# Performance work log

Hardware: AMD Instinct MI355X
Metric: run time of the kernel (lower is better)

Reference implementation:

```python
import jax, jax.numpy as jnp
import numpy as np

N = 50000   # nodes
E = 600000  # edges
D = 128     # in_feats
H = 128     # n_hidden
C = 47      # n_classes


def setup_inputs() -> dict:
    key = jax.random.key(0)
    ks = jax.random.split(key, 12)
    x = jax.random.normal(ks[0], (N, D), dtype=jnp.float32)
    src = jax.random.randint(ks[1], (E,), 0, N, dtype=jnp.int32)
    dst = jax.random.randint(ks[2], (E,), 0, N, dtype=jnp.int32)
    def lin(k, fi, fo):
        s = 1.0 / np.sqrt(fi)
        return jax.random.uniform(k, (fi, fo), jnp.float32, -s, s)
    return {
        "x": x, "src": src, "dst": dst,
        "W_self0": lin(ks[3], D, H), "W_neigh0": lin(ks[4], D, H), "b0": jnp.zeros((H,), jnp.float32),
        "W_self1": lin(ks[5], H, H), "W_neigh1": lin(ks[6], H, H), "b1": jnp.zeros((H,), jnp.float32),
        "W_self2": lin(ks[7], H, C), "W_neigh2": lin(ks[8], H, C), "b2": jnp.zeros((C,), jnp.float32),
    }


def _sage_layer(h, src, dst, W_self, W_neigh, b, act):
    # gather neighbor (src) features, mean-aggregate onto dst nodes
    msum = jax.ops.segment_sum(h[src], dst, num_segments=N)           # [N, F]
    deg = jax.ops.segment_sum(jnp.ones((src.shape[0], 1), h.dtype), dst, num_segments=N)
    h_neigh = msum / jnp.maximum(deg, 1.0)                            # zero-degree -> 0
    out = h @ W_self + h_neigh @ W_neigh + b
    return jax.nn.relu(out) if act else out


def reference(x, src, dst, W_self0, W_neigh0, b0, W_self1, W_neigh1, b1, W_self2, W_neigh2, b2):
    h = _sage_layer(x, src, dst, W_self0, W_neigh0, b0, True)
    h = _sage_layer(h, src, dst, W_self1, W_neigh1, b1, True)
    h = _sage_layer(h, src, dst, W_self2, W_neigh2, b2, False)
    return h
```

## Files before the change

### kernel.cpp

```cpp
#include <hip/hip_runtime.h>
#include <hip/hip_bf16.h>


#define THREADS 256

typedef unsigned short u16;
typedef __attribute__((ext_vector_type(8))) short bf16x8;
typedef __attribute__((ext_vector_type(4))) float f32x4;

__device__ inline u16 f2bf(float f) {
    union { float f; unsigned u; } v; v.f = f;
    unsigned r = (v.u + 0x7FFFu + ((v.u >> 16) & 1u)) >> 16;
    return (u16)r;
}
__device__ inline float bf2f(u16 b) {
    union { unsigned u; float f; } v; v.u = ((unsigned)b) << 16;
    return v.f;
}
__device__ inline unsigned pack2(float a, float b) {
    return (unsigned)f2bf(a) | ((unsigned)f2bf(b) << 16);
}

#define GLDS16(gp, lp)                                                         \
    __builtin_amdgcn_global_load_lds(                                          \
        (const __attribute__((address_space(1))) void*)(gp),                   \
        (__attribute__((address_space(3))) void*)(lp), 16, 0, 0)

__global__ void k_preamble(const float* __restrict__ x, u16* __restrict__ hi,
                           u16* __restrict__ lo, int n32,
                           const int* __restrict__ dst, int* __restrict__ deg, int E,
                           const float* __restrict__ Ws0, const float* __restrict__ Wn0,
                           const float* __restrict__ Ws1, const float* __restrict__ Wn1,
                           const float* __restrict__ Ws2, const float* __restrict__ Wn2,
                           u16* __restrict__ Bt) {
    int idx = blockIdx.x * blockDim.x + threadIdx.x;
    if (idx < n32) {
        float4 v = ((const float4*)x)[idx];
        float h0 = bf2f(f2bf(v.x)), h1 = bf2f(f2bf(v.y)), h2 = bf2f(f2bf(v.z)), h3 = bf2f(f2bf(v.w));
        uint2 hp, lp;
        hp.x = pack2(h0, h1); hp.y = pack2(h2, h3);
        lp.x = pack2(v.x - h0, v.y - h1); lp.y = pack2(v.z - h2, v.w - h3);
        ((uint2*)hi)[idx] = hp;
        ((uint2*)lo)[idx] = lp;
    }
    if (idx < E) atomicAdd(&deg[dst[idx]], 1);
    if (idx < 3 * 128 * 256) {
        int layer = idx >> 15;
        int within = idx & 32767;
        int col = within >> 8;
        int k = within & 255;
        const float* Ws = (layer == 0) ? Ws0 : (layer == 1) ? Ws1 : Ws2;
        const float* Wn = (layer == 0) ? Wn0 : (layer == 1) ? Wn1 : Wn2;
        int fout = (layer == 2) ? 47 : 128;
        float v = 0.f;
        if (col < fout) v = (k < 128) ? Ws[k * fout + col] : Wn[(k - 128) * fout + col];
        u16 h = f2bf(v);
        Bt[layer * 65536 + within] = h;
        Bt[layer * 65536 + 32768 + within] = f2bf(v - bf2f(h));
    }
}

__global__ void k_scan_block(const int* __restrict__ deg, int* __restrict__ off,
                             int* __restrict__ bsum, int n) {
    __shared__ int s[256];
    int t = threadIdx.x;
    int base = blockIdx.x * 1024 + t * 4;
    int v[4];
#pragma unroll
    for (int i = 0; i < 4; i++) v[i] = (base + i < n) ? deg[base + i] : 0;
    int sum = v[0] + v[1] + v[2] + v[3];
    int val = sum;
    s[t] = val;
    __syncthreads();
    for (int o = 1; o < 256; o <<= 1) {
        int x = (t >= o) ? s[t - o] : 0;
        __syncthreads();
        val += x;
        s[t] = val;
        __syncthreads();
    }
    int run = val - sum;
#pragma unroll
    for (int i = 0; i < 4; i++) {
        if (base + i < n) off[base + i] = run;
        run += v[i];
    }
    if (t == 255) bsum[blockIdx.x] = val;
}

__global__ void k_scan_add(int* __restrict__ off, const int* __restrict__ bsum, int n) {
    __shared__ int sAdd;
    int t = threadIdx.x;
    if (t < 64) {
        int v = 0;
        for (int i = t; i < blockIdx.x; i += 64) v += bsum[i];
#pragma unroll
        for (int o = 32; o; o >>= 1) v += __shfl_xor(v, o, 64);
        if (t == 0) sAdd = v;
    }
    __syncthreads();
    int add = sAdd;
    int base = blockIdx.x * 1024 + t * 4;
#pragma unroll
    for (int i = 0; i < 4; i++)
        if (base + i < n) off[base + i] += add;
}

__global__ void k_fill(const int* __restrict__ src, const int* __restrict__ dst,
                       const int* __restrict__ off, int* __restrict__ cur,
                       int* __restrict__ eidx, int E) {
    int e = blockIdx.x * blockDim.x + threadIdx.x;
    if (e < E) {
        int d = dst[e];
        int p = atomicAdd(&cur[d], 1);
        eidx[off[d] + p] = src[e];
    }
}

__global__ void k_aggregate(const u16* __restrict__ hi_in, const int* __restrict__ eidx,
                            const int* __restrict__ off, const int* __restrict__ deg,
                            u16* __restrict__ mhi, u16* __restrict__ mlo, int n) {
    int wv = blockIdx.x * 4 + (threadIdx.x >> 6);
    int lane = threadIdx.x & 63;
    int quarter = lane >> 4;
    int ql = lane & 15;
    int node = wv * 4 + quarter;
    if (node >= n) return;
    int cnt = deg[node];
    int base = off[node];
    const uint4* h4 = (const uint4*)hi_in;
    float acc[8];
#pragma unroll
    for (int i = 0; i < 8; i++) acc[i] = 0.f;
    for (int j = 0; j < cnt; j += 8) {
        int s[8];
        float m[8];
#pragma unroll
        for (int u = 0; u < 8; u++) {
            int jj = j + u;
            s[u] = eidx[base + (jj < cnt ? jj : 0)];
            m[u] = (jj < cnt) ? 1.f : 0.f;
        }
        uint4 v[8];
#pragma unroll
        for (int u = 0; u < 8; u++) v[u] = h4[(size_t)s[u] * 16 + ql];
#pragma unroll
        for (int u = 0; u < 8; u++) {
            acc[0] = fmaf(m[u], bf2f((u16)(v[u].x & 0xffffu)), acc[0]);
            acc[1] = fmaf(m[u], bf2f((u16)(v[u].x >> 16)), acc[1]);
            acc[2] = fmaf(m[u], bf2f((u16)(v[u].y & 0xffffu)), acc[2]);
            acc[3] = fmaf(m[u], bf2f((u16)(v[u].y >> 16)), acc[3]);
            acc[4] = fmaf(m[u], bf2f((u16)(v[u].z & 0xffffu)), acc[4]);
            acc[5] = fmaf(m[u], bf2f((u16)(v[u].z >> 16)), acc[5]);
            acc[6] = fmaf(m[u], bf2f((u16)(v[u].w & 0xffffu)), acc[6]);
            acc[7] = fmaf(m[u], bf2f((u16)(v[u].w >> 16)), acc[7]);
        }
    }
    float iv = 1.0f / (float)(cnt > 1 ? cnt : 1);
    float a[8], r[8];
#pragma unroll
    for (int i = 0; i < 8; i++) {
        a[i] = acc[i] * iv;
        r[i] = bf2f(f2bf(a[i]));
    }
    uint4 hp, lp;
    hp.x = pack2(a[0], a[1]); hp.y = pack2(a[2], a[3]);
    hp.z = pack2(a[4], a[5]); hp.w = pack2(a[6], a[7]);
    lp.x = pack2(a[0] - r[0], a[1] - r[1]); lp.y = pack2(a[2] - r[2], a[3] - r[3]);
    lp.z = pack2(a[4] - r[4], a[5] - r[5]); lp.w = pack2(a[6] - r[6], a[7] - r[7]);
    ((uint4*)mhi)[(size_t)node * 16 + ql] = hp;
    ((uint4*)mlo)[(size_t)node * 16 + ql] = lp;
}

__global__ __launch_bounds__(256) void k_gemm_mfma(
    const u16* __restrict__ Ahi_s, const u16* __restrict__ Alo_s,
    const u16* __restrict__ Ahi_n, const u16* __restrict__ Alo_n,
    const u16* __restrict__ Bthi, const u16* __restrict__ Btlo,
    const float* __restrict__ bias, float* __restrict__ out_f32,
    u16* __restrict__ out_hi, u16* __restrict__ out_lo, int n, int fout, int relu) {
    __shared__ u16 sAhi[64 * 32];
    __shared__ u16 sAlo[64 * 32];
    __shared__ u16 sBhi[128 * 32];
    __shared__ u16 sBlo[128 * 32];

    int t = threadIdx.x;
    int w = t >> 6;
    int lane = t & 63;
    int wr = w >> 1, wc = w & 1;
    size_t row0 = (size_t)blockIdx.x * 64;

    const bool slim = (fout <= 64);
    const int rbase = slim ? (w * 16) : (wr * 32);
    const int nR = slim ? 1 : 2;
    const int cbase = slim ? 0 : (wc * 64);

    f32x4 acc[2][4];
#pragma unroll
    for (int r = 0; r < 2; r++)
#pragma unroll
        for (int c = 0; c < 4; c++) acc[r][c] = (f32x4){0.f, 0.f, 0.f, 0.f};

    for (int kk = 0; kk < 256; kk += 32) {
        const u16* Phi = (kk < 128) ? Ahi_s : Ahi_n;
        const u16* Plo = (kk < 128) ? Alo_s : Alo_n;
        int kc = kk & 127;
        __syncthreads();
        {
            int r = w * 16 + (lane >> 2);
            int cb = (lane & 3) * 8;
            GLDS16(Phi + (row0 + r) * 128 + kc + cb, &sAhi[r * 32 + cb]);
            GLDS16(Plo + (row0 + r) * 128 + kc + cb, &sAlo[r * 32 + cb]);
        }
#pragma unroll
        for (int i = 0; i < 2; i++) {
            int c = w * 32 + i * 16 + (lane >> 2);
            int cb = (lane & 3) * 8;
            GLDS16(Bthi + (size_t)c * 256 + kk + cb, &sBhi[c * 32 + cb]);
            GLDS16(Btlo + (size_t)c * 256 + kk + cb, &sBlo[c * 32 + cb]);
        }
        __syncthreads();

        bf16x8 a_hi[2], a_lo[2], b_hi[4], b_lo[4];
        int q8 = (lane >> 4) * 8;
#pragma unroll
        for (int r = 0; r < 2; r++) {
            if (r >= nR) continue;
            int ad = (rbase + r * 16 + (lane & 15)) * 32 + q8;
            a_hi[r] = *(const bf16x8*)&sAhi[ad];
            a_lo[r] = *(const bf16x8*)&sAlo[ad];
        }
#pragma unroll
        for (int c = 0; c < 4; c++) {
            int ad = (cbase + c * 16 + (lane & 15)) * 32 + q8;
            b_hi[c] = *(const bf16x8*)&sBhi[ad];
            b_lo[c] = *(const bf16x8*)&sBlo[ad];
        }
#pragma unroll
        for (int r = 0; r < 2; r++) {
            if (r >= nR) continue;
#pragma unroll
            for (int c = 0; c < 4; c++) {
                acc[r][c] = __builtin_amdgcn_mfma_f32_16x16x32_bf16(
                    a_hi[r], b_hi[c], acc[r][c], 0, 0, 0);
                acc[r][c] = __builtin_amdgcn_mfma_f32_16x16x32_bf16(
                    a_hi[r], b_lo[c], acc[r][c], 0, 0, 0);
                acc[r][c] = __builtin_amdgcn_mfma_f32_16x16x32_bf16(
                    a_lo[r], b_hi[c], acc[r][c], 0, 0, 0);
            }
        }
    }

    int quad = lane >> 4;
    int lcol = lane & 15;
#pragma unroll
    for (int r = 0; r < 2; r++) {
        if (r >= nR) continue;
#pragma unroll
        for (int c = 0; c < 4; c++) {
            int col = cbase + c * 16 + lcol;
            float bv = (col < fout) ? bias[col] : 0.f;
#pragma unroll
            for (int g = 0; g < 4; g++) {
                size_t row = row0 + rbase + r * 16 + quad * 4 + g;
                if (row >= (size_t)n || col >= fout) continue;
                float v = acc[r][c][g] + bv;
                if (relu) v = v > 0.f ? v : 0.f;
                if (out_f32) out_f32[row * fout + col] = v;
                if (out_hi) {
                    u16 h = f2bf(v);
                    out_hi[row * 128 + col] = h;
                    out_lo[row * 128 + col] = f2bf(v - bf2f(h));
                }
            }
        }
    }
}

extern "C" void kernel_launch(void* const* d_in, const int* in_sizes, int n_in,
                              void* d_out, int out_size, void* d_ws, size_t ws_size,
                              hipStream_t stream) {
    const float* x = (const float*)d_in[0];
    const int* src = (const int*)d_in[1];
    const int* dst = (const int*)d_in[2];
    const float* Ws0 = (const float*)d_in[3];
    const float* Wn0 = (const float*)d_in[4];
    const float* b0 = (const float*)d_in[5];
    const float* Ws1 = (const float*)d_in[6];
    const float* Wn1 = (const float*)d_in[7];
    const float* b1 = (const float*)d_in[8];
    const float* Ws2 = (const float*)d_in[9];
    const float* Wn2 = (const float*)d_in[10];
    const float* b2 = (const float*)d_in[11];
    float* out = (float*)d_out;

    const int N = in_sizes[0] / 128;
    const int E = in_sizes[1];
    const int Npad = ((N + 63) / 64) * 64;

    char* p = (char*)d_ws;
    u16* P0hi = (u16*)p; p += (size_t)Npad * 128 * 2;
    u16* P0lo = (u16*)p; p += (size_t)Npad * 128 * 2;
    u16* P1hi = (u16*)p; p += (size_t)Npad * 128 * 2;
    u16* P1lo = (u16*)p; p += (size_t)Npad * 128 * 2;
    u16* Mhi = (u16*)p; p += (size_t)Npad * 128 * 2;
    u16* Mlo = (u16*)p; p += (size_t)Npad * 128 * 2;
    u16* Bt = (u16*)p; p += 3 * 2 * 128 * 256 * 2;
    int* deg = (int*)p; p += (size_t)N * 4;
    int* cur = (int*)p; p += (size_t)N * 4;
    int* off = (int*)p; p += (size_t)N * 4;
    int* eidx = (int*)p; p += (size_t)E * 4;
    int* bsum = (int*)p;

    const int nPX = N * 32;
    int nPre = nPX;
    if (E > nPre) nPre = E;
    if (3 * 128 * 256 > nPre) nPre = 3 * 128 * 256;
    const int nbPre = (nPre + THREADS - 1) / THREADS;
    const int nbE = (E + THREADS - 1) / THREADS;
    const int nbScan = (N + 1023) / 1024;
    const int nbAgg = (N + 15) / 16;
    const int nbGemm = (N + 63) / 64;

    hipMemsetAsync(deg, 0, (size_t)2 * N * sizeof(int), stream);

    k_preamble<<<nbPre, THREADS, 0, stream>>>(x, P0hi, P0lo, nPX, dst, deg, E,
                                              Ws0, Wn0, Ws1, Wn1, Ws2, Wn2, Bt);
    k_scan_block<<<nbScan, 256, 0, stream>>>(deg, off, bsum, N);
    k_scan_add<<<nbScan, 256, 0, stream>>>(off, bsum, N);
    k_fill<<<nbE, THREADS, 0, stream>>>(src, dst, off, cur, eidx, E);

    k_aggregate<<<nbAgg, 256, 0, stream>>>(P0hi, eidx, off, deg, Mhi, Mlo, N);
    k_gemm_mfma<<<nbGemm, 256, 0, stream>>>(P0hi, P0lo, Mhi, Mlo,
                                            Bt + 0 * 65536, Bt + 0 * 65536 + 32768, b0,
                                            (float*)nullptr, P1hi, P1lo, N, 128, 1);
    k_aggregate<<<nbAgg, 256, 0, stream>>>(P1hi, eidx, off, deg, Mhi, Mlo, N);
    k_gemm_mfma<<<nbGemm, 256, 0, stream>>>(P1hi, P1lo, Mhi, Mlo,
                                            Bt + 1 * 65536, Bt + 1 * 65536 + 32768, b1,
                                            (float*)nullptr, P0hi, P0lo, N, 128, 1);
    k_aggregate<<<nbAgg, 256, 0, stream>>>(P0hi, eidx, off, deg, Mhi, Mlo, N);
    k_gemm_mfma<<<nbGemm, 256, 0, stream>>>(P0hi, P0lo, Mhi, Mlo,
                                            Bt + 2 * 65536, Bt + 2 * 65536 + 32768, b2,
                                            out, (u16*)nullptr, (u16*)nullptr, N, 47, 0);
}
```

Before: 299.0 us.

## Enlarge GEMM row tile to 128 and XOR-swizzle LDS layout

Doubles the rows per GEMM block from 64 to 128, so each wave computes four row fragments and each weight tile loaded into LDS is reused across twice as many rows. It also XOR-swizzles the 16-byte chunks in the shared-memory A and B tiles to reduce bank conflicts on the fragment reads. This costs more accumulator registers and more LDS per block, which may lower occupancy, and the grid has half as many blocks. Padding of the node dimension is raised to match the new tile height.

```diff
diff --git a/kernel.cpp b/kernel.cpp
--- a/kernel.cpp
+++ b/kernel.cpp
@@ -178,8 +178,8 @@
     const u16* __restrict__ Bthi, const u16* __restrict__ Btlo,
     const float* __restrict__ bias, float* __restrict__ out_f32,
     u16* __restrict__ out_hi, u16* __restrict__ out_lo, int n, int fout, int relu) {
-    __shared__ u16 sAhi[64 * 32];
-    __shared__ u16 sAlo[64 * 32];
+    __shared__ u16 sAhi[128 * 32];
+    __shared__ u16 sAlo[128 * 32];
     __shared__ u16 sBhi[128 * 32];
     __shared__ u16 sBlo[128 * 32];
 
@@ -187,56 +187,63 @@
     int w = t >> 6;
     int lane = t & 63;
     int wr = w >> 1, wc = w & 1;
-    size_t row0 = (size_t)blockIdx.x * 64;
+    size_t row0 = (size_t)blockIdx.x * 128;
 
     const bool slim = (fout <= 64);
-    const int rbase = slim ? (w * 16) : (wr * 32);
-    const int nR = slim ? 1 : 2;
+    const int rbase = slim ? (w * 32) : (wr * 64);
+    const int nR = slim ? 2 : 4;
     const int cbase = slim ? 0 : (wc * 64);
 
-    f32x4 acc[2][4];
-#pragma unroll
-    for (int r = 0; r < 2; r++)
+    f32x4 acc[4][4];
+#pragma unroll
+    for (int r = 0; r < 4; r++)
 #pragma unroll
         for (int c = 0; c < 4; c++) acc[r][c] = (f32x4){0.f, 0.f, 0.f, 0.f};
+
+    int fr = lane & 15;
+    int q = lane >> 4;
 
     for (int kk = 0; kk < 256; kk += 32) {
         const u16* Phi = (kk < 128) ? Ahi_s : Ahi_n;
         const u16* Plo = (kk < 128) ? Alo_s : Alo_n;
         int kc = kk & 127;
         __syncthreads();
-        {
-            int r = w * 16 + (lane >> 2);
-            int cb = (lane & 3) * 8;
-            GLDS16(Phi + (row0 + r) * 128 + kc + cb, &sAhi[r * 32 + cb]);
-            GLDS16(Plo + (row0 + r) * 128 + kc + cb, &sAlo[r * 32 + cb]);
-        }
 #pragma unroll
         for (int i = 0; i < 2; i++) {
-            int c = w * 32 + i * 16 + (lane >> 2);
-            int cb = (lane & 3) * 8;
-            GLDS16(Bthi + (size_t)c * 256 + kk + cb, &sBhi[c * 32 + cb]);
-            GLDS16(Btlo + (size_t)c * 256 + kk + cb, &sBlo[c * 32 + cb]);
+            int r = (t >> 2) + i * 64;
+            int s = t & 3;
+            int sg = s ^ ((r >> 1) & 3);
+            GLDS16(Phi + (row0 + r) * 128 + kc + sg * 8, &sAhi[r * 32 + s * 8]);
+            GLDS16(Plo + (row0 + r) * 128 + kc + sg * 8, &sAlo[r * 32 + s * 8]);
+        }
+#pragma unroll
+        for (int i = 0; i < 2; i++) {
+            int c = (t >> 2) + i * 64;
+            int s = t & 3;
+            int sg = s ^ ((c >> 1) & 3);
+            GLDS16(Bthi + (size_t)c * 256 + kk + sg * 8, &sBhi[c * 32 + s * 8]);
+            GLDS16(Btlo + (size_t)c * 256 + kk + sg * 8, &sBlo[c * 32 + s * 8]);
         }
         __syncthreads();
 
-        bf16x8 a_hi[2], a_lo[2], b_hi[4], b_lo[4];
-        int q8 = (lane >> 4) * 8;
-#pragma unroll
-        for (int r = 0; r < 2; r++) {
+        bf16x8 a_hi[4], a_lo[4], b_hi[4], b_lo[4];
+#pragma unroll
+        for (int r = 0; r < 4; r++) {
             if (r >= nR) continue;
-            int ad = (rbase + r * 16 + (lane & 15)) * 32 + q8;
+            int row = rbase + r * 16 + fr;
+            int ad = row * 32 + ((q ^ ((row >> 1) & 3)) << 3);
             a_hi[r] = *(const bf16x8*)&sAhi[ad];
             a_lo[r] = *(const bf16x8*)&sAlo[ad];
         }
 #pragma unroll
         for (int c = 0; c < 4; c++) {
-            int ad = (cbase + c * 16 + (lane & 15)) * 32 + q8;
+            int col = cbase + c * 16 + fr;
+            int ad = col * 32 + ((q ^ ((col >> 1) & 3)) << 3);
             b_hi[c] = *(const bf16x8*)&sBhi[ad];
             b_lo[c] = *(const bf16x8*)&sBlo[ad];
         }
 #pragma unroll
-        for (int r = 0; r < 2; r++) {
+        for (int r = 0; r < 4; r++) {
             if (r >= nR) continue;
 #pragma unroll
             for (int c = 0; c < 4; c++) {
@@ -253,7 +260,7 @@
     int quad = lane >> 4;
     int lcol = lane & 15;
 #pragma unroll
-    for (int r = 0; r < 2; r++) {
+    for (int r = 0; r < 4; r++) {
         if (r >= nR) continue;
 #pragma unroll
         for (int c = 0; c < 4; c++) {
@@ -295,7 +302,7 @@
 
     const int N = in_sizes[0] / 128;
     const int E = in_sizes[1];
-    const int Npad = ((N + 63) / 64) * 64;
+    const int Npad = ((N + 127) / 128) * 128;
 
     char* p = (char*)d_ws;
     u16* P0hi = (u16*)p; p += (size_t)Npad * 128 * 2;
@@ -319,7 +326,7 @@
     const int nbE = (E + THREADS - 1) / THREADS;
     const int nbScan = (N + 1023) / 1024;
     const int nbAgg = (N + 15) / 16;
-    const int nbGemm = (N + 63) / 64;
+    const int nbGemm = (N + 127) / 128;
 
     hipMemsetAsync(deg, 0, (size_t)2 * N * sizeof(int), stream);
 
```

After: 306.8 us. +2.6%, slower.
